# Kernel optimization log

Measured on AMD Instinct MI355X. Metric: run time of the kernel, lower is better.

## Reference

```python
import jax, jax.numpy as jnp
import numpy as np
import math

EMB = 1024
HEADS = 16
VOCAB = 32000


def gelu_tanh(x):
    c = math.sqrt(2.0 / math.pi)
    return 0.5 * x * (1.0 + jnp.tanh(c * (x + 0.044715 * x * x * x)))


def layernorm(x, w, b, eps=1e-5):
    mean = jnp.mean(x, axis=-1, keepdims=True)
    var = jnp.var(x, axis=-1, keepdims=True)  # unbiased=False
    return w * ((x - mean) / jnp.sqrt(var + eps)) + b


def setup_inputs() -> dict:
    key = jax.random.key(0)
    ks = jax.random.split(key, 12)
    E, H, V = EMB, HEADS, VOCAB
    s = 1.0 / math.sqrt(E)
    return {
        "x": jax.random.normal(ks[0], (2, 2048, E), dtype=jnp.float32),
        "W_q": jax.random.normal(ks[1], (E, E), dtype=jnp.float32) * s,
        "W_k": jax.random.normal(ks[2], (E, E), dtype=jnp.float32) * s,
        "W_v": jax.random.normal(ks[3], (E, E), dtype=jnp.float32) * s,
        "ln1_w": jnp.ones((E,), jnp.float32),
        "ln1_b": jnp.zeros((E,), jnp.float32),
        "ln2_w": jnp.ones((E,), jnp.float32),
        "ln2_b": jnp.zeros((E,), jnp.float32),
        "ff_w1": jax.random.normal(ks[4], (E, 4 * E), dtype=jnp.float32) * s,
        "ff_b1": jnp.zeros((4 * E,), jnp.float32),
        "ff_w2": jax.random.normal(ks[5], (4 * E, E), dtype=jnp.float32) * (0.5 * s),
        "ff_b2": jnp.zeros((E,), jnp.float32),
        "proj_w": jax.random.normal(ks[6], (E, V), dtype=jnp.float32) * s,
        "proj_b": jnp.zeros((V,), jnp.float32),
    }


def attention(x, W_q, W_k, W_v):
    B, S, E = x.shape
    H = HEADS
    D = E // H
    q = (x @ W_q).reshape(B, S, H, D).transpose(0, 2, 1, 3)  # [B,H,S,D]
    k = (x @ W_k).reshape(B, S, H, D).transpose(0, 2, 1, 3)
    v = (x @ W_v).reshape(B, S, H, D).transpose(0, 2, 1, 3)
    scores = jnp.einsum("bhqd,bhkd->bhqk", q, k) / math.sqrt(D)
    causal = jnp.tril(jnp.ones((S, S), dtype=bool))
    scores = jnp.where(causal[None, None], scores, -jnp.inf)
    w = jax.nn.softmax(scores, axis=-1)
    ctx = jnp.einsum("bhqk,bhkd->bhqd", w, v)
    return ctx.transpose(0, 2, 1, 3).reshape(B, S, E)


def reference(x, W_q, W_k, W_v, ln1_w, ln1_b, ln2_w, ln2_b,
              ff_w1, ff_b1, ff_w2, ff_b2, proj_w, proj_b):
    # pre-LN attention block (dropout = identity, drop_rate=0)
    h = x + attention(layernorm(x, ln1_w, ln1_b), W_q, W_k, W_v)
    # pre-LN FFN block
    ff_in = layernorm(h, ln2_w, ln2_b)
    ff = gelu_tanh(ff_in @ ff_w1 + ff_b1) @ ff_w2 + ff_b2
    h = h + ff
    return h @ proj_w + proj_b
```

## Files before the change

### kernel.cpp

```cpp
#include <hip/hip_runtime.h>

using u16 = unsigned short;
typedef __attribute__((ext_vector_type(8))) short bf16x8;
typedef __attribute__((ext_vector_type(4))) float f32x4;

#define DEVI __device__ __forceinline__

DEVI float bf2f(u16 u){ union{ unsigned v; float f; } x; x.v = ((unsigned)u)<<16; return x.f; }
DEVI u16 f2bf(float f){ union{ float f; unsigned v; } x; x.f = f;
  unsigned r = x.v + 0x7FFFu + ((x.v>>16)&1u); return (u16)(r>>16); }

DEVI float gelu_f(float x){
  float y = 0.7978845608028654f*(x + 0.044715f*x*x*x);
  y = fminf(fmaxf(y, -30.f), 30.f);
  float e = __expf(2.f*y);
  return 0.5f*x*(1.f + (e-1.f)/(e+1.f));
}

DEVI void gload_lds16(const void* g, void* l){
  __builtin_amdgcn_global_load_lds((const __attribute__((address_space(1))) void*)g,
                                   (__attribute__((address_space(3))) void*)l, 16, 0, 0);
}

#define BARM asm volatile("s_barrier" ::: "memory")
#define LGKM0 asm volatile("s_waitcnt lgkmcnt(0)" ::: "memory")
#define VM8  asm volatile("s_waitcnt vmcnt(8)"  ::: "memory")
#define VM0  asm volatile("s_waitcnt vmcnt(0)"  ::: "memory")

__global__ __launch_bounds__(256) void wconv_kernel(const float* __restrict__ in,
                                                    u16* __restrict__ out, int R, int C){
  __shared__ u16 t[32][33];
  int c0 = blockIdx.x*32, r0 = blockIdx.y*32;
  int tc = threadIdx.x & 31, tr = threadIdx.x >> 5;
  #pragma unroll
  for (int i=0;i<4;i++){
    int r = tr + i*8;
    t[r][tc] = f2bf(in[(size_t)(r0+r)*C + (c0+tc)]);
  }
  __syncthreads();
  #pragma unroll
  for (int i=0;i<4;i++){
    int r = tr + i*8;
    out[(size_t)(c0+r)*R + (r0+tc)] = t[tc][r];
  }
}

DEVI void block_reduce2(float& s1, float& s2, int tid){
  #pragma unroll
  for (int off=1; off<64; off<<=1){ s1 += __shfl_xor(s1, off); s2 += __shfl_xor(s2, off); }
  __shared__ float red[8];
  int wid = tid>>6;
  if ((tid&63)==0){ red[wid*2]=s1; red[wid*2+1]=s2; }
  __syncthreads();
  s1 = red[0]+red[2]+red[4]+red[6];
  s2 = red[1]+red[3]+red[5]+red[7];
}

__global__ __launch_bounds__(256) void ln_kernel(const float* __restrict__ x,
    const float* __restrict__ w, const float* __restrict__ b, u16* __restrict__ out){
  int row = blockIdx.x, tid = threadIdx.x;
  float4 v = ((const float4*)(x + (size_t)row*1024))[tid];
  float s1 = v.x+v.y+v.z+v.w;
  float s2 = v.x*v.x+v.y*v.y+v.z*v.z+v.w*v.w;
  block_reduce2(s1,s2,tid);
  float mean = s1*(1.f/1024.f);
  float var  = s2*(1.f/1024.f) - mean*mean;
  float inv  = rsqrtf(var + 1e-5f);
  float4 wv = ((const float4*)w)[tid];
  float4 bv = ((const float4*)b)[tid];
  ushort4 o;
  o.x = f2bf(wv.x*((v.x-mean)*inv)+bv.x);
  o.y = f2bf(wv.y*((v.y-mean)*inv)+bv.y);
  o.z = f2bf(wv.z*((v.z-mean)*inv)+bv.z);
  o.w = f2bf(wv.w*((v.w-mean)*inv)+bv.w);
  ((ushort4*)(out + (size_t)row*1024))[tid] = o;
}

__global__ __launch_bounds__(256) void resln_kernel(const float* __restrict__ x,
    const u16* __restrict__ ctx, const float* __restrict__ w, const float* __restrict__ b,
    float* __restrict__ h, u16* __restrict__ hb){
  int row = blockIdx.x, tid = threadIdx.x;
  float4 xv = ((const float4*)(x + (size_t)row*1024))[tid];
  ushort4 cv = ((const ushort4*)(ctx + (size_t)row*1024))[tid];
  float4 hv;
  hv.x = xv.x + bf2f(cv.x); hv.y = xv.y + bf2f(cv.y);
  hv.z = xv.z + bf2f(cv.z); hv.w = xv.w + bf2f(cv.w);
  ((float4*)(h + (size_t)row*1024))[tid] = hv;
  float s1 = hv.x+hv.y+hv.z+hv.w;
  float s2 = hv.x*hv.x+hv.y*hv.y+hv.z*hv.z+hv.w*hv.w;
  block_reduce2(s1,s2,tid);
  float mean = s1*(1.f/1024.f);
  float var  = s2*(1.f/1024.f) - mean*mean;
  float inv  = rsqrtf(var + 1e-5f);
  float4 wv = ((const float4*)w)[tid];
  float4 bv = ((const float4*)b)[tid];
  ushort4 o;
  o.x = f2bf(wv.x*((hv.x-mean)*inv)+bv.x);
  o.y = f2bf(wv.y*((hv.y-mean)*inv)+bv.y);
  o.z = f2bf(wv.z*((hv.z-mean)*inv)+bv.z);
  o.w = f2bf(wv.w*((hv.w-mean)*inv)+bv.w);
  ((ushort4*)(hb + (size_t)row*1024))[tid] = o;
}

template<class EpiF>
DEVI void gemm8_core(const u16* __restrict__ A, const u16* __restrict__ Bt,
                     int K, int m0, int n0, EpiF epi){
  __shared__ __align__(16) u16 As[2][16384];
  __shared__ __align__(16) u16 Bs[2][16384];
  const int tid = threadIdx.x;
  const int wid = tid>>6, lane = tid&63;
  const int wr = wid>>2, wc = wid&3;
  const int g = lane>>4, l16 = lane&15;
  const int wq = wid&3;
  const int lr = lane>>3, ls = lane&7;

  f32x4 acc[8][4] = {};

  const u16* aSrc[2][2]; unsigned aDst[2][2];
  #pragma unroll
  for (int qm=0;qm<2;qm++)
    #pragma unroll
    for (int j=0;j<2;j++){
      int r = wr*128 + qm*64 + wq*16 + j*8 + lr;
      aSrc[qm][j] = A + (size_t)(m0 + r)*K + ((ls ^ (r&7))*8);
      aDst[qm][j] = (unsigned)(((wr*128 + qm*64)*8 + (wq*2+j)*64)*16);
    }
  const u16* bSrc[2][2]; unsigned bDst[2][2];
  #pragma unroll
  for (int qn=0;qn<2;qn++)
    #pragma unroll
    for (int j=0;j<2;j++){
      int r = wc*64 + qn*32 + wr*16 + j*8 + lr;
      bSrc[qn][j] = Bt + (size_t)(n0 + r)*K + ((ls ^ (r&7))*8);
      bDst[qn][j] = (unsigned)(((wc*64 + qn*32)*8 + (wr*2+j)*64)*16);
    }

  auto stageAll = [&](int buf, int kc){
    char* ab = (char*)&As[buf][0];
    char* bb = (char*)&Bs[buf][0];
    #pragma unroll
    for (int j=0;j<2;j++) gload_lds16(aSrc[0][j] + kc, ab + aDst[0][j]);
    #pragma unroll
    for (int j=0;j<2;j++) gload_lds16(bSrc[0][j] + kc, bb + bDst[0][j]);
    #pragma unroll
    for (int j=0;j<2;j++) gload_lds16(bSrc[1][j] + kc, bb + bDst[1][j]);
    #pragma unroll
    for (int j=0;j<2;j++) gload_lds16(aSrc[1][j] + kc, ab + aDst[1][j]);
  };
  auto ldA = [&](int buf, int qm, bf16x8 (&a)[4][2]){
    const char* base = (const char*)&As[buf][0];
    #pragma unroll
    for (int i=0;i<4;i++){
      int r = wr*128 + qm*64 + i*16 + l16;
      #pragma unroll
      for (int kk=0;kk<2;kk++)
        a[i][kk] = *(const bf16x8*)(base + r*128 + ((kk*64 + g*16) ^ ((l16&7)<<4)));
    }
  };
  auto ldB = [&](int buf, int qn, bf16x8 (&b)[2][2]){
    const char* base = (const char*)&Bs[buf][0];
    #pragma unroll
    for (int i=0;i<2;i++){
      int r = wc*64 + qn*32 + i*16 + l16;
      #pragma unroll
      for (int kk=0;kk<2;kk++)
        b[i][kk] = *(const bf16x8*)(base + r*128 + ((kk*64 + g*16) ^ ((l16&7)<<4)));
    }
  };
  auto mm = [&](int qm, int qn, bf16x8 (&a)[4][2], bf16x8 (&b)[2][2]){
    __builtin_amdgcn_s_setprio(1);
    #pragma unroll
    for (int i=0;i<4;i++)
      #pragma unroll
      for (int n=0;n<2;n++)
        #pragma unroll
        for (int kk=0;kk<2;kk++)
          acc[qm*4+i][qn*2+n] =
            __builtin_amdgcn_mfma_f32_16x16x32_bf16(a[i][kk], b[n][kk], acc[qm*4+i][qn*2+n], 0,0,0);
    __builtin_amdgcn_s_setprio(0);
  };

  const int NT = K>>6;
  stageAll(0, 0);
  stageAll(1, 64);

  bf16x8 a[4][2], b0[2][2], b1[2][2];
  int cur = 0;
  for (int t=0; t<NT; ++t){
    if (t < NT-1) { VM8; } else { VM0; }
    BARM;
    ldA(cur,0,a); ldB(cur,0,b0); ldB(cur,1,b1);
    mm(0,0,a,b0);
    mm(0,1,a,b1);
    ldA(cur,1,a);
    LGKM0; BARM;
    if (t+2 < NT) stageAll(cur, (t+2)<<6);
    mm(1,0,a,b0);
    mm(1,1,a,b1);
    cur ^= 1;
  }
  BARM;
  epi((char*)&As[0][0], (char*)&Bs[0][0], acc);
}

DEVI int xcd_swz(int id, int nwg){ return (id&7)*(nwg>>3) + (id>>3); }

__global__ __launch_bounds__(512,2) void proj8_kernel(const u16* __restrict__ hfb,
    const u16* __restrict__ pwt, const float* __restrict__ pb, float* __restrict__ out){
  const int xcd = blockIdx.x & 7, c = blockIdx.x >> 3;
  const int mt = 2*xcd + (c & 1);
  const int nt = c >> 1;
  const int m0 = mt*256, n0 = nt*256;
  gemm8_core(hfb, pwt, 1024, m0, n0,
    [&](char* sA, char* sB, f32x4 (&acc)[8][4]){
      const int tid = threadIdx.x;
      const int wid = tid>>6, lane = tid&63;
      const int wr = wid>>2, wc = wid&3;
      const int g = lane>>4, l16 = lane&15;
      float* ep = (float*)((wid<4 ? sA : sB) + (wid&3)*16384);
      float bb[4];
      #pragma unroll
      for (int nf=0;nf<4;nf++) bb[nf] = pb[n0 + wc*64 + nf*16 + l16];
      #pragma unroll
      for (int p=0;p<2;p++){
        #pragma unroll
        for (int mf4=0;mf4<4;mf4++){
          int mf = p*4 + mf4;
          #pragma unroll
          for (int nf=0;nf<4;nf++){
            #pragma unroll
            for (int r=0;r<4;r++)
              ep[(mf4*16 + g*4 + r)*64 + nf*16 + l16] = acc[mf][nf][r] + bb[nf];
          }
        }
        LGKM0;
        #pragma unroll
        for (int it=0;it<16;it++){
          int rl = it*4 + g;
          f32x4 v = *(const f32x4*)&ep[rl*64 + l16*4];
          int grow = m0 + wr*128 + p*64 + rl;
          *(f32x4*)&out[(size_t)grow*32000 + n0 + wc*64 + l16*4] = v;
        }
        LGKM0;
      }
    });
}

__global__ __launch_bounds__(512,2) void ffn1_8_kernel(const u16* __restrict__ hb,
    const u16* __restrict__ w1t, const float* __restrict__ b1, u16* __restrict__ gout){
  int swz = xcd_swz(blockIdx.x, gridDim.x);
  int mt = swz & 15, nt = swz >> 4;
  const int m0 = mt*256, n0 = nt*256;
  gemm8_core(hb, w1t, 1024, m0, n0,
    [&](char*, char*, f32x4 (&acc)[8][4]){
      const int tid = threadIdx.x;
      const int wid = tid>>6, lane = tid&63;
      const int wr = wid>>2, wc = wid&3;
      const int g = lane>>4, l16 = lane&15;
      #pragma unroll
      for (int mf=0;mf<8;mf++)
        #pragma unroll
        for (int nf=0;nf<4;nf++){
          int row = m0 + wr*128 + mf*16 + g*4;
          int col = n0 + wc*64 + nf*16 + l16;
          float bb = b1[col];
          #pragma unroll
          for (int r=0;r<4;r++)
            gout[(size_t)(row+r)*4096 + col] = f2bf(gelu_f(acc[mf][nf][r] + bb));
        }
    });
}

__global__ __launch_bounds__(512,2) void qkv8_kernel(const u16* __restrict__ xn,
    const u16* __restrict__ wqt, const u16* __restrict__ wkt, const u16* __restrict__ wvt,
    u16* __restrict__ qo, u16* __restrict__ ko, u16* __restrict__ vo){
  int swz = xcd_swz(blockIdx.x, gridDim.x);
  int mt = swz & 15, ntt = swz >> 4;
  int sel = ntt >> 2;
  const u16* Bt = (sel==0)?wqt:((sel==1)?wkt:wvt);
  u16* outp = (sel==0)?qo:((sel==1)?ko:vo);
  const int m0 = mt*256, n0 = (ntt&3)*256;
  gemm8_core(xn, Bt, 1024, m0, n0,
    [&](char*, char*, f32x4 (&acc)[8][4]){
      const int tid = threadIdx.x;
      const int wid = tid>>6, lane = tid&63;
      const int wr = wid>>2, wc = wid&3;
      const int g = lane>>4, l16 = lane&15;
      #pragma unroll
      for (int mf=0;mf<8;mf++)
        #pragma unroll
        for (int nf=0;nf<4;nf++){
          int row = m0 + wr*128 + mf*16 + g*4;
          int col = n0 + wc*64 + nf*16 + l16;
          #pragma unroll
          for (int r=0;r<4;r++)
            outp[(size_t)(row+r)*1024 + col] = f2bf(acc[mf][nf][r]);
        }
    });
}

template<int BM,int BN,int WM,int WN, class EpiF>
DEVI void gemm_core(const u16* __restrict__ A, const u16* __restrict__ Bt,
                    int K, int m0, int n0, EpiF epi){
  constexpr int WAVES_N = BN/WN;
  static_assert((BM/WM)*(BN/WN) == 4, "4 waves");
  constexpr int FM = WM/16, FN = WN/16;
  __shared__ u16 As[2][BM*32];
  __shared__ u16 Bs[2][BN*32];
  const int tid = threadIdx.x;
  const int wid = tid>>6, lane = tid&63;
  const int wr = wid / WAVES_N, wc = wid % WAVES_N;
  const int g = lane>>4, l16 = lane&15;
  f32x4 acc[FM][FN] = {};

  auto stage = [&](int buf, int t){
    #pragma unroll
    for (int j=0;j<BM/64;j++){
      int cbase = wid*BM + j*64;
      int c = cbase + lane;
      int r = c>>2, c4 = c&3;
      gload_lds16(A + (size_t)(m0+r)*K + t*32 + c4*8, &As[buf][cbase*8]);
    }
    #pragma unroll
    for (int j=0;j<BN/64;j++){
      int cbase = wid*BN + j*64;
      int c = cbase + lane;
      int r = c>>2, c4 = c&3;
      gload_lds16(Bt + (size_t)(n0+r)*K + t*32 + c4*8, &Bs[buf][cbase*8]);
    }
  };

  const int NT = K/32;
  stage(0,0);
  __syncthreads();
  for (int t=0;t<NT;t++){
    int cur = t&1;
    if (t+1 < NT) stage(cur^1, t+1);
    bf16x8 a[FM], b[FN];
    #pragma unroll
    for (int m=0;m<FM;m++) a[m] = *(const bf16x8*)&As[cur][(wr*WM + m*16 + l16)*32 + g*8];
    #pragma unroll
    for (int n=0;n<FN;n++) b[n] = *(const bf16x8*)&Bs[cur][(wc*WN + n*16 + l16)*32 + g*8];
    #pragma unroll
    for (int m=0;m<FM;m++)
      #pragma unroll
      for (int n=0;n<FN;n++)
        acc[m][n] = __builtin_amdgcn_mfma_f32_16x16x32_bf16(a[m], b[n], acc[m][n], 0,0,0);
    __syncthreads();
  }
  #pragma unroll
  for (int m=0;m<FM;m++)
    #pragma unroll
    for (int n=0;n<FN;n++){
      int row = m0 + wr*WM + m*16 + g*4;
      int col = n0 + wc*WN + n*16 + l16;
      epi(row, col, acc[m][n]);
    }
}

__global__ __launch_bounds__(256) void ffn2_kernel(const u16* __restrict__ gin,
    const u16* __restrict__ w2t, const float* __restrict__ b2,
    const float* __restrict__ h, u16* __restrict__ hfb){
  gemm_core<64,128,32,64>(gin, w2t, 4096, blockIdx.x*64, blockIdx.y*128,
    [&](int row,int col,f32x4 v){
      #pragma unroll
      for (int r=0;r<4;r++){
        float t = h[(size_t)(row+r)*1024 + col] + v[r] + b2[col];
        hfb[(size_t)(row+r)*1024 + col] = f2bf(t);
      }
    });
}

__global__ __launch_bounds__(256) void attn_kernel(const u16* __restrict__ q,
    const u16* __restrict__ k, const u16* __restrict__ v, u16* __restrict__ ctx){
  __shared__ u16 Qs[64*64], Ks[64*64], Vt[64*64];
  __shared__ u16 Ps[4][16*64];
  const int tid = threadIdx.x, lane = tid&63, wid = tid>>6;
  const int g = lane>>4, l16 = lane&15;
  const int b = blockIdx.x>>4, hh = blockIdx.x&15;
  const int qb = blockIdx.y;
  const size_t tokbase = (size_t)b*2048;
  const int hoff = hh*64;

  #pragma unroll
  for (int j=0;j<2;j++){
    int c = j*256 + tid;
    int r = c>>3, c8 = c&7;
    uint4 val = *(const uint4*)(q + (tokbase + qb*64 + r)*1024 + hoff + c8*8);
    *(uint4*)((char*)Qs + r*128 + ((c8*16) ^ ((r&7)<<4))) = val;
  }
  __syncthreads();
  bf16x8 qa[2];
  const int qrow_l = wid*16 + l16;
  #pragma unroll
  for (int kk=0;kk<2;kk++)
    qa[kk] = *(const bf16x8*)((const char*)Qs + qrow_l*128 + ((kk*64 + g*16) ^ ((qrow_l&7)<<4)));

  float m_r[4], l_r[4];
  f32x4 o_acc[4] = {};
  #pragma unroll
  for (int r=0;r<4;r++){ m_r[r] = -1e30f; l_r[r] = 0.f; }

  for (int kt=0; kt<=qb; kt++){
    __syncthreads();
    const int kv0 = kt*64;
    #pragma unroll
    for (int j=0;j<2;j++){
      int c = j*256 + tid;
      int r = c>>3, c8 = c&7;
      uint4 val = *(const uint4*)(k + (tokbase + kv0 + r)*1024 + hoff + c8*8);
      *(uint4*)((char*)Ks + r*128 + ((c8*16) ^ ((r&7)<<4))) = val;
    }
    #pragma unroll
    for (int j=0;j<2;j++){
      int c = j*256 + tid;
      int kv = c>>3, d8 = c&7;
      union{ uint4 u; u16 s[8]; } uu;
      uu.u = *(const uint4*)(v + (tokbase + kv0 + kv)*1024 + hoff + d8*8);
      #pragma unroll
      for (int e=0;e<8;e++){
        int d = d8*8+e;
        *(u16*)((char*)Vt + d*128 + ((kv*2) ^ ((d&7)<<4))) = uu.s[e];
      }
    }
    __syncthreads();

    f32x4 s[4] = {};
    #pragma unroll
    for (int c=0;c<4;c++){
      #pragma unroll
      for (int kk=0;kk<2;kk++){
        int krow = c*16 + l16;
        bf16x8 kb = *(const bf16x8*)((const char*)Ks + krow*128 + ((kk*64 + g*16) ^ ((krow&7)<<4)));
        s[c] = __builtin_amdgcn_mfma_f32_16x16x32_bf16(qa[kk], kb, s[c], 0,0,0);
      }
    }
    const int qrow0 = qb*64 + wid*16 + g*4;
    float sv[4][4];
    #pragma unroll
    for (int c=0;c<4;c++){
      #pragma unroll
      for (int r=0;r<4;r++){
        float xx = s[c][r] * 0.125f;
        if (kt==qb){
          int kvabs = kv0 + c*16 + l16;
          if (kvabs > qrow0 + r) xx = -1e30f;
        }
        sv[c][r] = xx;
      }
    }
    #pragma unroll
    for (int r=0;r<4;r++){
      float rm = fmaxf(fmaxf(sv[0][r],sv[1][r]),fmaxf(sv[2][r],sv[3][r]));
      #pragma unroll
      for (int off=1; off<16; off<<=1) rm = fmaxf(rm, __shfl_xor(rm, off));
      float mn  = fmaxf(m_r[r], rm);
      float fac = __expf(m_r[r] - mn);
      float rs = 0.f;
      const int prow = g*4 + r;
      #pragma unroll
      for (int c=0;c<4;c++){
        float p = __expf(sv[c][r] - mn);
        rs += p;
        *(u16*)((char*)&Ps[wid][0] + prow*128 + (((c*16+l16)*2) ^ ((prow&7)<<4))) = f2bf(p);
      }
      #pragma unroll
      for (int off=1; off<16; off<<=1) rs += __shfl_xor(rs, off);
      m_r[r] = mn;
      l_r[r] = l_r[r]*fac + rs;
      #pragma unroll
      for (int c=0;c<4;c++) o_acc[c][r] *= fac;
    }
    bf16x8 pa[2];
    #pragma unroll
    for (int kk=0;kk<2;kk++)
      pa[kk] = *(const bf16x8*)((const char*)&Ps[wid][0] + l16*128 + ((kk*64 + g*16) ^ ((l16&7)<<4)));
    #pragma unroll
    for (int c=0;c<4;c++){
      #pragma unroll
      for (int kk=0;kk<2;kk++){
        int vrow = c*16 + l16;
        bf16x8 vb = *(const bf16x8*)((const char*)Vt + vrow*128 + ((kk*64 + g*16) ^ ((vrow&7)<<4)));
        o_acc[c] = __builtin_amdgcn_mfma_f32_16x16x32_bf16(pa[kk], vb, o_acc[c], 0,0,0);
      }
    }
  }
  #pragma unroll
  for (int c=0;c<4;c++){
    #pragma unroll
    for (int r=0;r<4;r++){
      float o = o_acc[c][r] / l_r[r];
      size_t tok = tokbase + qb*64 + wid*16 + g*4 + r;
      ctx[tok*1024 + hoff + c*16 + l16] = f2bf(o);
    }
  }
}

extern "C" void kernel_launch(void* const* d_in, const int* in_sizes, int n_in,
                              void* d_out, int out_size, void* d_ws, size_t ws_size,
                              hipStream_t stream){
  (void)in_sizes; (void)n_in; (void)out_size; (void)ws_size;
  const float* x    = (const float*)d_in[0];
  const float* Wq   = (const float*)d_in[1];
  const float* Wk   = (const float*)d_in[2];
  const float* Wv   = (const float*)d_in[3];
  const float* ln1w = (const float*)d_in[4];
  const float* ln1b = (const float*)d_in[5];
  const float* ln2w = (const float*)d_in[6];
  const float* ln2b = (const float*)d_in[7];
  const float* fw1  = (const float*)d_in[8];
  const float* fb1  = (const float*)d_in[9];
  const float* fw2  = (const float*)d_in[10];
  const float* fb2  = (const float*)d_in[11];
  const float* pw   = (const float*)d_in[12];
  const float* pb   = (const float*)d_in[13];

  char* ob = (char*)d_out;
  u16* wqt = (u16*)(ob + 0);
  u16* wkt = (u16*)(ob + 2097152);
  u16* wvt = (u16*)(ob + 4194304);
  u16* w1t = (u16*)(ob + 6291456);
  u16* w2t = (u16*)(ob + 14680064);
  u16* xn  = (u16*)(ob + 23068672);
  u16* qbf = (u16*)(ob + 31457280);
  u16* kbf = (u16*)(ob + 39845888);
  u16* vbf = (u16*)(ob + 48234496);
  u16* ctx = (u16*)(ob + 56623104);
  float* h = (float*)(ob + 65011712);
  u16* hb  = (u16*)(ob + 81788928);
  u16* gbuf= (u16*)(ob + 90177536);

  char* wsb = (char*)d_ws;
  u16* pwt = (u16*)(wsb + 0);
  u16* hfb = (u16*)(wsb + 65536000);

  wconv_kernel<<<dim3(32,32)  ,256,0,stream>>>(Wq , wqt, 1024, 1024);
  wconv_kernel<<<dim3(32,32)  ,256,0,stream>>>(Wk , wkt, 1024, 1024);
  wconv_kernel<<<dim3(32,32)  ,256,0,stream>>>(Wv , wvt, 1024, 1024);
  wconv_kernel<<<dim3(128,32) ,256,0,stream>>>(fw1, w1t, 1024, 4096);
  wconv_kernel<<<dim3(32,128) ,256,0,stream>>>(fw2, w2t, 4096, 1024);
  wconv_kernel<<<dim3(1000,32),256,0,stream>>>(pw , pwt, 1024, 32000);

  ln_kernel    <<<4096,256,0,stream>>>(x, ln1w, ln1b, xn);
  qkv8_kernel  <<<192,512,0,stream>>>(xn, wqt, wkt, wvt, qbf, kbf, vbf);
  attn_kernel  <<<dim3(32,32),256,0,stream>>>(qbf, kbf, vbf, ctx);
  resln_kernel <<<4096,256,0,stream>>>(x, ctx, ln2w, ln2b, h, hb);
  ffn1_8_kernel<<<256,512,0,stream>>>(hb, w1t, fb1, gbuf);
  ffn2_kernel  <<<dim3(64,8) ,256,0,stream>>>(gbuf, w2t, fb2, h, hfb);
  proj8_kernel <<<2000,512,0,stream>>>(hfb, pwt, pb, (float*)d_out);
}
```

Baseline: 708.0 us.

## Shrink GEMM tiles from 256x256/8-wave to 128x128/4-wave blocks

```diff
diff --git a/kernel.cpp b/kernel.cpp
--- a/kernel.cpp
+++ b/kernel.cpp
@@ -103,198 +103,180 @@
 }
 
 template<class EpiF>
-DEVI void gemm8_core(const u16* __restrict__ A, const u16* __restrict__ Bt,
-                     int K, int m0, int n0, EpiF epi){
-  __shared__ __align__(16) u16 As[2][16384];
-  __shared__ __align__(16) u16 Bs[2][16384];
+DEVI void gemm128_core(const u16* __restrict__ A, const u16* __restrict__ Bt,
+                       int K, int m0, int n0, EpiF epi){
+  __shared__ __align__(16) u16 As[2][8192];
+  __shared__ __align__(16) u16 Bs[2][8192];
   const int tid = threadIdx.x;
   const int wid = tid>>6, lane = tid&63;
-  const int wr = wid>>2, wc = wid&3;
+  const int wr = wid>>1, wc = wid&1;
   const int g = lane>>4, l16 = lane&15;
-  const int wq = wid&3;
   const int lr = lane>>3, ls = lane&7;
 
-  f32x4 acc[8][4] = {};
-
-  const u16* aSrc[2][2]; unsigned aDst[2][2];
-  #pragma unroll
-  for (int qm=0;qm<2;qm++)
-    #pragma unroll
-    for (int j=0;j<2;j++){
-      int r = wr*128 + qm*64 + wq*16 + j*8 + lr;
-      aSrc[qm][j] = A + (size_t)(m0 + r)*K + ((ls ^ (r&7))*8);
-      aDst[qm][j] = (unsigned)(((wr*128 + qm*64)*8 + (wq*2+j)*64)*16);
-    }
-  const u16* bSrc[2][2]; unsigned bDst[2][2];
-  #pragma unroll
-  for (int qn=0;qn<2;qn++)
-    #pragma unroll
-    for (int j=0;j<2;j++){
-      int r = wc*64 + qn*32 + wr*16 + j*8 + lr;
-      bSrc[qn][j] = Bt + (size_t)(n0 + r)*K + ((ls ^ (r&7))*8);
-      bDst[qn][j] = (unsigned)(((wc*64 + qn*32)*8 + (wr*2+j)*64)*16);
-    }
+  f32x4 acc[4][4] = {};
+
+  const u16* aSrc[4]; unsigned aDst[4];
+  const u16* bSrc[4]; unsigned bDst[4];
+  #pragma unroll
+  for (int j=0;j<4;j++){
+    int r = wid*32 + j*8 + lr;
+    aSrc[j] = A  + (size_t)(m0 + r)*K + ((ls ^ lr)*8);
+    bSrc[j] = Bt + (size_t)(n0 + r)*K + ((ls ^ lr)*8);
+    aDst[j] = (unsigned)((wid*32 + j*8)*128);
+    bDst[j] = aDst[j];
+  }
 
   auto stageAll = [&](int buf, int kc){
     char* ab = (char*)&As[buf][0];
     char* bb = (char*)&Bs[buf][0];
     #pragma unroll
-    for (int j=0;j<2;j++) gload_lds16(aSrc[0][j] + kc, ab + aDst[0][j]);
-    #pragma unroll
-    for (int j=0;j<2;j++) gload_lds16(bSrc[0][j] + kc, bb + bDst[0][j]);
-    #pragma unroll
-    for (int j=0;j<2;j++) gload_lds16(bSrc[1][j] + kc, bb + bDst[1][j]);
-    #pragma unroll
-    for (int j=0;j<2;j++) gload_lds16(aSrc[1][j] + kc, ab + aDst[1][j]);
+    for (int j=0;j<4;j++) gload_lds16(aSrc[j] + kc, ab + aDst[j]);
+    #pragma unroll
+    for (int j=0;j<4;j++) gload_lds16(bSrc[j] + kc, bb + bDst[j]);
   };
-  auto ldA = [&](int buf, int qm, bf16x8 (&a)[4][2]){
+  auto ldA = [&](int buf, bf16x8 (&a)[4][2]){
     const char* base = (const char*)&As[buf][0];
     #pragma unroll
     for (int i=0;i<4;i++){
-      int r = wr*128 + qm*64 + i*16 + l16;
+      int r = wr*64 + i*16 + l16;
       #pragma unroll
       for (int kk=0;kk<2;kk++)
         a[i][kk] = *(const bf16x8*)(base + r*128 + ((kk*64 + g*16) ^ ((l16&7)<<4)));
     }
   };
-  auto ldB = [&](int buf, int qn, bf16x8 (&b)[2][2]){
+  auto ldB = [&](int buf, bf16x8 (&b)[4][2]){
     const char* base = (const char*)&Bs[buf][0];
     #pragma unroll
-    for (int i=0;i<2;i++){
-      int r = wc*64 + qn*32 + i*16 + l16;
+    for (int i=0;i<4;i++){
+      int r = wc*64 + i*16 + l16;
       #pragma unroll
       for (int kk=0;kk<2;kk++)
         b[i][kk] = *(const bf16x8*)(base + r*128 + ((kk*64 + g*16) ^ ((l16&7)<<4)));
     }
-  };
-  auto mm = [&](int qm, int qn, bf16x8 (&a)[4][2], bf16x8 (&b)[2][2]){
-    __builtin_amdgcn_s_setprio(1);
-    #pragma unroll
-    for (int i=0;i<4;i++)
-      #pragma unroll
-      for (int n=0;n<2;n++)
-        #pragma unroll
-        for (int kk=0;kk<2;kk++)
-          acc[qm*4+i][qn*2+n] =
-            __builtin_amdgcn_mfma_f32_16x16x32_bf16(a[i][kk], b[n][kk], acc[qm*4+i][qn*2+n], 0,0,0);
-    __builtin_amdgcn_s_setprio(0);
   };
 
   const int NT = K>>6;
   stageAll(0, 0);
   stageAll(1, 64);
 
-  bf16x8 a[4][2], b0[2][2], b1[2][2];
+  bf16x8 a[4][2], b[4][2];
   int cur = 0;
   for (int t=0; t<NT; ++t){
     if (t < NT-1) { VM8; } else { VM0; }
     BARM;
-    ldA(cur,0,a); ldB(cur,0,b0); ldB(cur,1,b1);
-    mm(0,0,a,b0);
-    mm(0,1,a,b1);
-    ldA(cur,1,a);
+    ldA(cur, a); ldB(cur, b);
+    __builtin_amdgcn_s_setprio(1);
+    #pragma unroll
+    for (int i=0;i<2;i++)
+      #pragma unroll
+      for (int n=0;n<4;n++)
+        #pragma unroll
+        for (int kk=0;kk<2;kk++)
+          acc[i][n] = __builtin_amdgcn_mfma_f32_16x16x32_bf16(a[i][kk], b[n][kk], acc[i][n], 0,0,0);
+    __builtin_amdgcn_s_setprio(0);
     LGKM0; BARM;
     if (t+2 < NT) stageAll(cur, (t+2)<<6);
-    mm(1,0,a,b0);
-    mm(1,1,a,b1);
+    __builtin_amdgcn_s_setprio(1);
+    #pragma unroll
+    for (int i=2;i<4;i++)
+      #pragma unroll
+      for (int n=0;n<4;n++)
+        #pragma unroll
+        for (int kk=0;kk<2;kk++)
+          acc[i][n] = __builtin_amdgcn_mfma_f32_16x16x32_bf16(a[i][kk], b[n][kk], acc[i][n], 0,0,0);
+    __builtin_amdgcn_s_setprio(0);
     cur ^= 1;
   }
   BARM;
   epi((char*)&As[0][0], (char*)&Bs[0][0], acc);
 }
 
-DEVI int xcd_swz(int id, int nwg){ return (id&7)*(nwg>>3) + (id>>3); }
-
-__global__ __launch_bounds__(512,2) void proj8_kernel(const u16* __restrict__ hfb,
+__global__ __launch_bounds__(256,2) void proj8_kernel(const u16* __restrict__ hfb,
     const u16* __restrict__ pwt, const float* __restrict__ pb, float* __restrict__ out){
   const int xcd = blockIdx.x & 7, c = blockIdx.x >> 3;
-  const int mt = 2*xcd + (c & 1);
-  const int nt = c >> 1;
-  const int m0 = mt*256, n0 = nt*256;
-  gemm8_core(hfb, pwt, 1024, m0, n0,
-    [&](char* sA, char* sB, f32x4 (&acc)[8][4]){
+  const int mt = 4*xcd + (c & 3);
+  const int nt = c >> 2;
+  const int m0 = mt*128, n0 = nt*128;
+  gemm128_core(hfb, pwt, 1024, m0, n0,
+    [&](char* sA, char* sB, f32x4 (&acc)[4][4]){
       const int tid = threadIdx.x;
       const int wid = tid>>6, lane = tid&63;
-      const int wr = wid>>2, wc = wid&3;
+      const int wr = wid>>1, wc = wid&1;
       const int g = lane>>4, l16 = lane&15;
-      float* ep = (float*)((wid<4 ? sA : sB) + (wid&3)*16384);
+      float* ep = (float*)((wid<2 ? sA : sB) + (wid&1)*16384);
       float bb[4];
       #pragma unroll
       for (int nf=0;nf<4;nf++) bb[nf] = pb[n0 + wc*64 + nf*16 + l16];
       #pragma unroll
-      for (int p=0;p<2;p++){
+      for (int i=0;i<4;i++)
         #pragma unroll
-        for (int mf4=0;mf4<4;mf4++){
-          int mf = p*4 + mf4;
+        for (int nf=0;nf<4;nf++)
           #pragma unroll
-          for (int nf=0;nf<4;nf++){
-            #pragma unroll
-            for (int r=0;r<4;r++)
-              ep[(mf4*16 + g*4 + r)*64 + nf*16 + l16] = acc[mf][nf][r] + bb[nf];
-          }
-        }
-        LGKM0;
-        #pragma unroll
-        for (int it=0;it<16;it++){
-          int rl = it*4 + g;
-          f32x4 v = *(const f32x4*)&ep[rl*64 + l16*4];
-          int grow = m0 + wr*128 + p*64 + rl;
-          *(f32x4*)&out[(size_t)grow*32000 + n0 + wc*64 + l16*4] = v;
-        }
-        LGKM0;
+          for (int r=0;r<4;r++)
+            ep[(i*16 + g*4 + r)*64 + nf*16 + l16] = acc[i][nf][r] + bb[nf];
+      LGKM0;
+      #pragma unroll
+      for (int it=0;it<16;it++){
+        int rl = it*4 + g;
+        f32x4 v = *(const f32x4*)&ep[rl*64 + l16*4];
+        int grow = m0 + wr*64 + rl;
+        *(f32x4*)&out[(size_t)grow*32000 + n0 + wc*64 + l16*4] = v;
       }
     });
 }
 
-__global__ __launch_bounds__(512,2) void ffn1_8_kernel(const u16* __restrict__ hb,
+__global__ __launch_bounds__(256,2) void ffn1_8_kernel(const u16* __restrict__ hb,
     const u16* __restrict__ w1t, const float* __restrict__ b1, u16* __restrict__ gout){
-  int swz = xcd_swz(blockIdx.x, gridDim.x);
-  int mt = swz & 15, nt = swz >> 4;
-  const int m0 = mt*256, n0 = nt*256;
-  gemm8_core(hb, w1t, 1024, m0, n0,
-    [&](char*, char*, f32x4 (&acc)[8][4]){
+  const int xcd = blockIdx.x & 7, c = blockIdx.x >> 3;
+  const int mt = 4*xcd + (c & 3);
+  const int nt = c >> 2;
+  const int m0 = mt*128, n0 = nt*128;
+  gemm128_core(hb, w1t, 1024, m0, n0,
+    [&](char*, char*, f32x4 (&acc)[4][4]){
       const int tid = threadIdx.x;
       const int wid = tid>>6, lane = tid&63;
-      const int wr = wid>>2, wc = wid&3;
+      const int wr = wid>>1, wc = wid&1;
       const int g = lane>>4, l16 = lane&15;
       #pragma unroll
-      for (int mf=0;mf<8;mf++)
+      for (int i=0;i<4;i++)
         #pragma unroll
         for (int nf=0;nf<4;nf++){
-          int row = m0 + wr*128 + mf*16 + g*4;
+          int row = m0 + wr*64 + i*16 + g*4;
           int col = n0 + wc*64 + nf*16 + l16;
           float bb = b1[col];
           #pragma unroll
           for (int r=0;r<4;r++)
-            gout[(size_t)(row+r)*4096 + col] = f2bf(gelu_f(acc[mf][nf][r] + bb));
+            gout[(size_t)(row+r)*4096 + col] = f2bf(gelu_f(acc[i][nf][r] + bb));
         }
     });
 }
 
-__global__ __launch_bounds__(512,2) void qkv8_kernel(const u16* __restrict__ xn,
+__global__ __launch_bounds__(256,2) void qkv8_kernel(const u16* __restrict__ xn,
     const u16* __restrict__ wqt, const u16* __restrict__ wkt, const u16* __restrict__ wvt,
     u16* __restrict__ qo, u16* __restrict__ ko, u16* __restrict__ vo){
-  int swz = xcd_swz(blockIdx.x, gridDim.x);
-  int mt = swz & 15, ntt = swz >> 4;
-  int sel = ntt >> 2;
+  const int xcd = blockIdx.x & 7, c = blockIdx.x >> 3;
+  const int mt = 4*xcd + (c & 3);
+  const int rest = c >> 2;
+  const int sel = rest >> 3;
+  const int nt = rest & 7;
   const u16* Bt = (sel==0)?wqt:((sel==1)?wkt:wvt);
   u16* outp = (sel==0)?qo:((sel==1)?ko:vo);
-  const int m0 = mt*256, n0 = (ntt&3)*256;
-  gemm8_core(xn, Bt, 1024, m0, n0,
-    [&](char*, char*, f32x4 (&acc)[8][4]){
+  const int m0 = mt*128, n0 = nt*128;
+  gemm128_core(xn, Bt, 1024, m0, n0,
+    [&](char*, char*, f32x4 (&acc)[4][4]){
       const int tid = threadIdx.x;
       const int wid = tid>>6, lane = tid&63;
-      const int wr = wid>>2, wc = wid&3;
+      const int wr = wid>>1, wc = wid&1;
       const int g = lane>>4, l16 = lane&15;
       #pragma unroll
-      for (int mf=0;mf<8;mf++)
+      for (int i=0;i<4;i++)
         #pragma unroll
         for (int nf=0;nf<4;nf++){
-          int row = m0 + wr*128 + mf*16 + g*4;
+          int row = m0 + wr*64 + i*16 + g*4;
           int col = n0 + wc*64 + nf*16 + l16;
           #pragma unroll
           for (int r=0;r<4;r++)
-            outp[(size_t)(row+r)*1024 + col] = f2bf(acc[mf][nf][r]);
+            outp[(size_t)(row+r)*1024 + col] = f2bf(acc[i][nf][r]);
         }
     });
 }
@@ -542,10 +524,10 @@
   wconv_kernel<<<dim3(1000,32),256,0,stream>>>(pw , pwt, 1024, 32000);
 
   ln_kernel    <<<4096,256,0,stream>>>(x, ln1w, ln1b, xn);
-  qkv8_kernel  <<<192,512,0,stream>>>(xn, wqt, wkt, wvt, qbf, kbf, vbf);
+  qkv8_kernel  <<<768,256,0,stream>>>(xn, wqt, wkt, wvt, qbf, kbf, vbf);
   attn_kernel  <<<dim3(32,32),256,0,stream>>>(qbf, kbf, vbf, ctx);
   resln_kernel <<<4096,256,0,stream>>>(x, ctx, ln2w, ln2b, h, hb);
-  ffn1_8_kernel<<<256,512,0,stream>>>(hb, w1t, fb1, gbuf);
+  ffn1_8_kernel<<<1024,256,0,stream>>>(hb, w1t, fb1, gbuf);
   ffn2_kernel  <<<dim3(64,8) ,256,0,stream>>>(gbuf, w2t, fb2, h, hfb);
-  proj8_kernel <<<2000,512,0,stream>>>(hfb, pwt, pb, (float*)d_out);
-}
+  proj8_kernel <<<8000,256,0,stream>>>(hfb, pwt, pb, (float*)d_out);
+}
```

Measured after the change: 786.1 us. 11.0% more time.
